# Optimization experiments

Measured on AMD Instinct MI355X. Metric: run time of the kernel, lower is better.

## Reference

```python
import jax, jax.numpy as jnp
import numpy as np

STEP_SIZE = 0.3333          # module default self.step_size
N_STEPS = 4                 # >= ceil(halfWidth/step) for sigma=6, size_factor=1; extra steps are masked to 0
REF_SIZE = 1024.0           # IndexHelper.input_size_factor() reference resolution


def _bilinear(img, px, py):
    """Bilinear sample img [B,C,H,W] at normalized coords px,py [B,H,W] in [0,1].
    Pixel centers at (j+0.5)/W (grid_sample align_corners=False convention); border clamp."""
    B, C, H, W = img.shape
    fx = px * W - 0.5
    fy = py * H - 0.5
    x0 = jnp.floor(fx)
    y0 = jnp.floor(fy)
    wx = (fx - x0)[:, None]  # [B,1,H,W]
    wy = (fy - y0)[:, None]
    x0i = jnp.clip(x0.astype(jnp.int32), 0, W - 1)
    x1i = jnp.clip(x0i + 1, 0, W - 1)
    y0i = jnp.clip(y0.astype(jnp.int32), 0, H - 1)
    y1i = jnp.clip(y0i + 1, 0, H - 1)
    gather = jax.vmap(lambda im, yi, xi: im[:, yi, xi])  # per-batch advanced indexing -> [B,C,H,W]
    v00 = gather(img, y0i, x0i)
    v01 = gather(img, y0i, x1i)
    v10 = gather(img, y1i, x0i)
    v11 = gather(img, y1i, x1i)
    top = v00 * (1.0 - wx) + v01 * wx
    bot = v10 * (1.0 - wx) + v11 * wx
    return top * (1.0 - wy) + bot * wy


def _forward(x, tangent, sigma):
    B, C, H, W = x.shape
    dt = x.dtype
    size_factor = min(H, W) / REF_SIZE           # i.input_size_factor()
    sig = sigma.reshape(-1, 1, 1, 1) * size_factor  # precisionFactor = 1.0
    half_width = 2.0 * sig
    two_sigma2 = 2.0 * sig * sig
    step = 1.0 / (STEP_SIZE * size_factor)       # step = i.view(1/step_size), mode=None scaling

    # p_start: normalized pixel-center coords, channel 0 = x (width), channel 1 = y (height)
    ys, xs = jnp.meshgrid((jnp.arange(H, dtype=dt) + 0.5) / H,
                          (jnp.arange(W, dtype=dt) + 0.5) / W, indexing="ij")
    p_start = jnp.broadcast_to(jnp.stack([xs, ys])[None], (B, 2, H, W))
    tex = jnp.array([W, H], dtype=dt).reshape(1, 2, 1, 1)  # i.tex_size()

    def march(direction):
        v0 = direction
        p0 = p_start + v0 / tex

        def body(carry, it):
            c, c_sum, p, v = carry
            r = (it + 1.0) * step                       # r = step, step+step, ...
            k = jnp.exp(-r * r / two_sigma2)            # [B,1,1,1]
            k = jnp.where(r < half_width, k, 0.0)
            px, py = p[:, 0], p[:, 1]
            inb = (px >= 0.0) & (px < 1.0) & (py >= 0.0) & (py < 1.0)
            k = k * inb[:, None].astype(dt)             # [B,1,H,W]
            c = c + _bilinear(x, px, py) * k
            c_sum = c_sum + k
            tf = _bilinear(tangent, px, py)
            vt = jnp.sum(v * tf, axis=1, keepdims=True)
            tf = jnp.where(vt < 0.0, -tf, tf)           # keep marching direction consistent
            p = p + tf / tex
            return (c, c_sum, p, tf), None

        init = (jnp.zeros_like(x), jnp.zeros((B, 1, H, W), dt), p0, v0)
        (c, c_sum, _, _), _ = jax.lax.scan(body, init, jnp.arange(N_STEPS, dtype=dt))
        return c, c_sum

    c1, s1 = march(tangent)      # smoothed(C, Sum, tangent_sampled)
    c2, s2 = march(-tangent)     # smoothed(C, Sum, -tangent_sampled)
    return (x + c1 + c2) / (1.0 + s1 + s2)


def setup_inputs() -> dict:
    key = jax.random.key(0)
    k1, k2 = jax.random.split(key)
    B, C, H, W = 2, 3, 1024, 1024
    x = jax.random.normal(k1, (B, C, H, W), jnp.float32)
    # tangent: unit-length per-pixel flow direction field
    theta = jax.random.uniform(k2, (B, 1, H, W), jnp.float32, 0.0, 2.0 * np.pi)
    tangent = jnp.concatenate([jnp.cos(theta), jnp.sin(theta)], axis=1)
    sigma = jnp.full((B,), 6.0, jnp.float32)  # smoothing width in pixels
    return {"x": x, "tangent": tangent, "sigma": sigma}


def reference(x, tangent, sigma):
    return _forward(x, tangent, sigma)
```

## Files before the change

kernel.cpp:

```cpp
#include <hip/hip_runtime.h>

constexpr int Bb = 2, Cc = 3, Hh = 1024, Ww = 1024;
constexpr int HWp = Hh * Ww;
constexpr int TSX = 32, TSY = 8;
constexpr int HALO = 6;
constexpr int TDX = TSX + 2 * HALO;
constexpr int TDY = TSY + 2 * HALO;
constexpr int TSTR = 48;

struct Corn { int o00, o01, o10, o11; float wx, wy, omx, omy; };

__device__ __forceinline__ Corn mkcorn_int(float px, float py, int ox, int oy) {
#pragma clang fp contract(off)
    float fx = px - 0.5f;
    float fy = py - 0.5f;
    float fx0 = floorf(fx), fy0 = floorf(fy);
    Corn c;
    c.wx = fx - fx0;  c.wy = fy - fy0;
    c.omx = 1.0f - c.wx;  c.omy = 1.0f - c.wy;
    int o = ((int)fy0 - oy) * TSTR + ((int)fx0 - ox);
    c.o00 = o;        c.o01 = o + 1;
    c.o10 = o + TSTR; c.o11 = o + TSTR + 1;
    return c;
}

__device__ __forceinline__ Corn mkcorn_bor(float px, float py, int ox, int oy) {
#pragma clang fp contract(off)
    float fx = px - 0.5f;
    float fy = py - 0.5f;
    float fx0 = floorf(fx), fy0 = floorf(fy);
    Corn c;
    c.wx = fx - fx0;  c.wy = fy - fy0;
    c.omx = 1.0f - c.wx;  c.omy = 1.0f - c.wy;
    int x0 = (int)fx0, y0 = (int)fy0;
    int x0i = min(max(x0, 0), Ww - 1);
    int x1i = min(x0i + 1, Ww - 1);
    int y0i = min(max(y0, 0), Hh - 1);
    int y1i = min(y0i + 1, Hh - 1);
    int lx0 = x0i - ox, lx1 = x1i - ox;
    int ly0 = y0i - oy, ly1 = y1i - oy;
    c.o00 = ly0 * TSTR + lx0;  c.o01 = ly0 * TSTR + lx1;
    c.o10 = ly1 * TSTR + lx0;  c.o11 = ly1 * TSTR + lx1;
    return c;
}

template <bool BORDER>
__device__ __forceinline__ void run_tile(
    const float* __restrict__ x, const float* __restrict__ tg,
    const float* __restrict__ sg, float* __restrict__ out,
    float (&lds)[5][TDY * TSTR])
{
#pragma clang fp contract(off)
    const int tx0 = blockIdx.x * TSX, ty0 = blockIdx.y * TSY;
    const int b = blockIdx.z;
    const int tid = threadIdx.x;

    const float* xp  = x  + (size_t)b * Cc * HWp;
    const float* txp = tg + (size_t)b * 2 * HWp;
    const float* planes[5] = { xp, xp + HWp, xp + 2 * HWp, txp, txp + HWp };
    const int ox = tx0 - HALO, oy = ty0 - HALO;

    float sig = sg[b];
    float half_width = 2.0f * sig;
    float two_sigma2 = (2.0f * sig) * sig;
    const float stepf = (float)(1.0 / 0.3333);
    float kv[4];
#pragma unroll
    for (int it = 0; it < 4; ++it) {
        float r = ((float)it + 1.0f) * stepf;
        float k = expf(-(r * r) / two_sigma2);
        kv[it] = (r < half_width) ? k : 0.0f;
    }
    const float k0 = kv[0], k1 = kv[1], k2 = kv[2], k3 = kv[3];
    const int nlive = __builtin_amdgcn_readfirstlane(
        (k0 != 0.0f) + (k1 != 0.0f) + (k2 != 0.0f) + (k3 != 0.0f));

    if (!BORDER) {
        for (int e = tid; e < TDY * (TDX / 2); e += 256) {
            int r = e / (TDX / 2);
            int c2 = e - r * (TDX / 2);
            int g = (oy + r) * Ww + ox + 2 * c2;
            int d = r * TSTR + 2 * c2;
#pragma unroll
            for (int pl = 0; pl < 5; ++pl) {
                float2 v = *reinterpret_cast<const float2*>(planes[pl] + g);
                *reinterpret_cast<float2*>(&lds[pl][d]) = v;
            }
        }
    } else {
        for (int e = tid; e < TDY * TDX; e += 256) {
            int r = e / TDX, cc = e - r * TDX;
            int gy = min(max(oy + r, 0), Hh - 1);
            int gx = min(max(ox + cc, 0), Ww - 1);
            int g = gy * Ww + gx;
#pragma unroll
            for (int pl = 0; pl < 5; ++pl)
                lds[pl][r * TSTR + cc] = planes[pl][g];
        }
    }
    __syncthreads();

    const int lx = tid & (TSX - 1), ly = tid >> 5;
    const int j = tx0 + lx, i = ty0 + ly;
    const int ctr = (HALO + ly) * TSTR + (HALO + lx);

    const float psx = (float)j + 0.5f;
    const float psy = (float)i + 0.5f;

    const float v0x = lds[3][ctr];
    const float v0y = lds[4][ctr];

    float pxA = psx + v0x, pyA = psy + v0y, vxA = v0x, vyA = v0y;
    float pxB = psx - v0x, pyB = psy - v0y, vxB = -v0x, vyB = -v0y;
    float aA0 = 0.f, aA1 = 0.f, aA2 = 0.f, asA = 0.f;
    float aB0 = 0.f, aB1 = 0.f, aB2 = 0.f, asB = 0.f;

#define MKC(C, PX, PY)                                                      \
    Corn C = BORDER ? mkcorn_bor(PX, PY, ox, oy)                            \
                    : mkcorn_int(PX, PY, ox, oy)

#define COLORSTEP(C, PX, PY, KW, A0, A1, A2, AS) do {                       \
    float w_ = (KW);                                                        \
    if (BORDER) {                                                           \
        bool inb_ = ((PX) >= 0.0f) && ((PX) < 1024.0f) &&                   \
                    ((PY) >= 0.0f) && ((PY) < 1024.0f);                     \
        w_ = inb_ ? w_ : 0.0f;                                              \
    }                                                                       \
    float w00_ = C.omx * C.omy, w01_ = C.wx * C.omy;                        \
    float w10_ = C.omx * C.wy,  w11_ = C.wx * C.wy;                         \
    float s0_ = fmaf(w01_, lds[0][C.o01], w00_ * lds[0][C.o00]);            \
    s0_ = fmaf(w10_, lds[0][C.o10], s0_);                                   \
    s0_ = fmaf(w11_, lds[0][C.o11], s0_);                                   \
    A0 = fmaf(s0_, w_, A0);                                                 \
    float s1_ = fmaf(w01_, lds[1][C.o01], w00_ * lds[1][C.o00]);            \
    s1_ = fmaf(w10_, lds[1][C.o10], s1_);                                   \
    s1_ = fmaf(w11_, lds[1][C.o11], s1_);                                   \
    A1 = fmaf(s1_, w_, A1);                                                 \
    float s2_ = fmaf(w01_, lds[2][C.o01], w00_ * lds[2][C.o00]);            \
    s2_ = fmaf(w10_, lds[2][C.o10], s2_);                                   \
    s2_ = fmaf(w11_, lds[2][C.o11], s2_);                                   \
    A2 = fmaf(s2_, w_, A2);                                                 \
    AS += w_;                                                               \
} while (0)

#define ADVSTEP(C, PX, PY, VX, VY) do {                                     \
    float x00_ = lds[3][C.o00], x01_ = lds[3][C.o01];                       \
    float x10_ = lds[3][C.o10], x11_ = lds[3][C.o11];                       \
    float y00_ = lds[4][C.o00], y01_ = lds[4][C.o01];                       \
    float y10_ = lds[4][C.o10], y11_ = lds[4][C.o11];                       \
    float xt_ = x00_ * C.omx + x01_ * C.wx;                                 \
    float xb_ = x10_ * C.omx + x11_ * C.wx;                                 \
    float tfx_ = xt_ * C.omy + xb_ * C.wy;                                  \
    float yt_ = y00_ * C.omx + y01_ * C.wx;                                 \
    float yb_ = y10_ * C.omx + y11_ * C.wx;                                 \
    float tfy_ = yt_ * C.omy + yb_ * C.wy;                                  \
    float vt_ = ((VX) * tfx_) + ((VY) * tfy_);                              \
    if (vt_ < 0.0f) { tfx_ = -tfx_; tfy_ = -tfy_; }                         \
    PX = (PX) + tfx_;  PY = (PY) + tfy_;                                    \
    VX = tfx_;  VY = tfy_;                                                  \
} while (0)

    if (nlive >= 1) {
        MKC(cA0, pxA, pyA);  MKC(cB0, pxB, pyB);
        COLORSTEP(cA0, pxA, pyA, k0, aA0, aA1, aA2, asA);
        COLORSTEP(cB0, pxB, pyB, k0, aB0, aB1, aB2, asB);
        if (nlive >= 2) {
            ADVSTEP(cA0, pxA, pyA, vxA, vyA);
            ADVSTEP(cB0, pxB, pyB, vxB, vyB);
            MKC(cA1, pxA, pyA);  MKC(cB1, pxB, pyB);
            COLORSTEP(cA1, pxA, pyA, k1, aA0, aA1, aA2, asA);
            COLORSTEP(cB1, pxB, pyB, k1, aB0, aB1, aB2, asB);
            if (nlive >= 3) {
                ADVSTEP(cA1, pxA, pyA, vxA, vyA);
                ADVSTEP(cB1, pxB, pyB, vxB, vyB);
                MKC(cA2, pxA, pyA);  MKC(cB2, pxB, pyB);
                COLORSTEP(cA2, pxA, pyA, k2, aA0, aA1, aA2, asA);
                COLORSTEP(cB2, pxB, pyB, k2, aB0, aB1, aB2, asB);
                if (nlive >= 4) {
                    ADVSTEP(cA2, pxA, pyA, vxA, vyA);
                    ADVSTEP(cB2, pxB, pyB, vxB, vyB);
                    MKC(cA3, pxA, pyA);  MKC(cB3, pxB, pyB);
                    COLORSTEP(cA3, pxA, pyA, k3, aA0, aA1, aA2, asA);
                    COLORSTEP(cB3, pxB, pyB, k3, aB0, aB1, aB2, asB);
                }
            }
        }
    }
#undef MKC
#undef COLORSTEP
#undef ADVSTEP

    const int pix = i * Ww + j;
    float xc0 = lds[0][ctr], xc1 = lds[1][ctr], xc2 = lds[2][ctr];
    float denom = (1.0f + asA) + asB;
    float* op = out + (size_t)b * Cc * HWp;
    op[pix]           = ((xc0 + aA0) + aB0) / denom;
    op[pix + HWp]     = ((xc1 + aA1) + aB1) / denom;
    op[pix + 2 * HWp] = ((xc2 + aA2) + aB2) / denom;
}

__global__ __launch_bounds__(256, 8) void flow_smooth_kernel(
    const float* __restrict__ x,
    const float* __restrict__ tg,
    const float* __restrict__ sg,
    float* __restrict__ out)
{
    __shared__ float lds[5][TDY * TSTR];
    const bool border = (blockIdx.x == 0) || (blockIdx.x == gridDim.x - 1) ||
                        (blockIdx.y == 0) || (blockIdx.y == gridDim.y - 1);
    if (border) run_tile<true >(x, tg, sg, out, lds);
    else        run_tile<false>(x, tg, sg, out, lds);
}

extern "C" void kernel_launch(void* const* d_in, const int* in_sizes, int n_in,
                              void* d_out, int out_size, void* d_ws, size_t ws_size,
                              hipStream_t stream) {
    const float* x = nullptr; const float* tg = nullptr; const float* sg = nullptr;
    for (int t = 0; t < n_in; ++t) {
        if (in_sizes[t] == Bb * Cc * HWp)      x  = (const float*)d_in[t];
        else if (in_sizes[t] == Bb * 2 * HWp)  tg = (const float*)d_in[t];
        else                                   sg = (const float*)d_in[t];
    }
    float* out = (float*)d_out;

    dim3 block(256, 1, 1);
    dim3 grid(Ww / TSX, Hh / TSY, Bb);
    flow_smooth_kernel<<<grid, block, 0, stream>>>(x, tg, sg, out);
}
```

Before: 115.5 us.

## Shrink vertical halo and swizzle block order across XCDs

Trims the vertical halo from 6 to 5 rows, so each tile loads fewer LDS rows and less redundant global data. The launch also moves to a flat 1D grid whose block index is remapped, so consecutive hardware dispatch slots (spread round-robin over 8 XCDs) land on contiguous neighbouring tiles. The aim is better L2 reuse of halo data within each XCD. The risk is that a 5-row halo may not cover the maximum vertical reach of the march, which would read the wrong LDS entries.

```diff
diff --git a/kernel.cpp b/kernel.cpp
--- a/kernel.cpp
+++ b/kernel.cpp
@@ -3,9 +3,10 @@
 constexpr int Bb = 2, Cc = 3, Hh = 1024, Ww = 1024;
 constexpr int HWp = Hh * Ww;
 constexpr int TSX = 32, TSY = 8;
-constexpr int HALO = 6;
-constexpr int TDX = TSX + 2 * HALO;
-constexpr int TDY = TSY + 2 * HALO;
+constexpr int HALOX = 6;
+constexpr int HALOY = 5;
+constexpr int TDX = TSX + 2 * HALOX;
+constexpr int TDY = TSY + 2 * HALOY;
 constexpr int TSTR = 48;
 
 struct Corn { int o00, o01, o10, o11; float wx, wy, omx, omy; };
@@ -46,19 +47,19 @@
 
 template <bool BORDER>
 __device__ __forceinline__ void run_tile(
+    int bx, int by, int b,
     const float* __restrict__ x, const float* __restrict__ tg,
     const float* __restrict__ sg, float* __restrict__ out,
     float (&lds)[5][TDY * TSTR])
 {
 #pragma clang fp contract(off)
-    const int tx0 = blockIdx.x * TSX, ty0 = blockIdx.y * TSY;
-    const int b = blockIdx.z;
+    const int tx0 = bx * TSX, ty0 = by * TSY;
     const int tid = threadIdx.x;
 
     const float* xp  = x  + (size_t)b * Cc * HWp;
     const float* txp = tg + (size_t)b * 2 * HWp;
     const float* planes[5] = { xp, xp + HWp, xp + 2 * HWp, txp, txp + HWp };
-    const int ox = tx0 - HALO, oy = ty0 - HALO;
+    const int ox = tx0 - HALOX, oy = ty0 - HALOY;
 
     float sig = sg[b];
     float half_width = 2.0f * sig;
@@ -102,7 +103,7 @@
 
     const int lx = tid & (TSX - 1), ly = tid >> 5;
     const int j = tx0 + lx, i = ty0 + ly;
-    const int ctr = (HALO + ly) * TSTR + (HALO + lx);
+    const int ctr = (HALOY + ly) * TSTR + (HALOX + lx);
 
     const float psx = (float)j + 0.5f;
     const float psy = (float)i + 0.5f;
@@ -206,10 +207,17 @@
     float* __restrict__ out)
 {
     __shared__ float lds[5][TDY * TSTR];
-    const bool border = (blockIdx.x == 0) || (blockIdx.x == gridDim.x - 1) ||
-                        (blockIdx.y == 0) || (blockIdx.y == gridDim.y - 1);
-    if (border) run_tile<true >(x, tg, sg, out, lds);
-    else        run_tile<false>(x, tg, sg, out, lds);
+
+    const int fid = blockIdx.x;
+    const int swz = (fid & 7) * 1024 + (fid >> 3);
+    const int b  = swz >> 12;
+    const int rem = swz & 4095;
+    const int by = rem >> 5;
+    const int bx = rem & 31;
+
+    const bool border = (bx == 0) || (bx == 31) || (by == 0) || (by == 127);
+    if (border) run_tile<true >(bx, by, b, x, tg, sg, out, lds);
+    else        run_tile<false>(bx, by, b, x, tg, sg, out, lds);
 }
 
 extern "C" void kernel_launch(void* const* d_in, const int* in_sizes, int n_in,
@@ -224,6 +232,6 @@
     float* out = (float*)d_out;
 
     dim3 block(256, 1, 1);
-    dim3 grid(Ww / TSX, Hh / TSY, Bb);
+    dim3 grid(8192, 1, 1);
     flow_smooth_kernel<<<grid, block, 0, stream>>>(x, tg, sg, out);
 }
```

Result: no change. 114.6 us (-0.7%).
